# Kernel optimization log

Measured on AMD Instinct MI355X. Metric: run time of the kernel, lower is better.

The kernel has to match this reference:

```python
import jax, jax.numpy as jnp
import numpy as np

N_NODES = 50000
N_EDGES = 800000
BATCH = 8
IN_CH = 64
OUT_CH = 64
K = 6


def setup_inputs() -> dict:
    key = jax.random.key(0)
    k1, k2, k3, k4 = jax.random.split(key, 4)
    x = jax.random.normal(k1, (BATCH, N_NODES, IN_CH), dtype=jnp.float32)
    edge_index = jax.random.randint(k2, (2, N_EDGES), 0, N_NODES, dtype=jnp.int64)
    # small weights keep the order-K Chebyshev recursion numerically stable
    edge_weight = jax.random.normal(k3, (N_EDGES,), dtype=jnp.float32) * 0.05
    W = jax.random.normal(k4, (K, IN_CH, OUT_CH), dtype=jnp.float32) * (1.0 / np.sqrt(IN_CH))
    bias = jnp.zeros((OUT_CH,), dtype=jnp.float32)
    return {"x": x, "edge_index": edge_index, "edge_weight": edge_weight, "W": W, "bias": bias}


def _spmm(edge_index, edge_weight, x, n_nodes):
    # sparse Laplacian @ x for batched features x: [B, N, C]
    src = edge_index[1]  # gather column
    dst = edge_index[0]  # scatter row
    msg = x[:, src, :] * edge_weight[None, :, None]      # [B, E, C]
    agg = jax.ops.segment_sum(msg.transpose(1, 0, 2), dst, num_segments=n_nodes)  # [N, B, C]
    return agg.transpose(1, 0, 2)                        # [B, N, C]


def reference(x, edge_index, edge_weight, W, bias):
    n = x.shape[1]
    t_prev = x                                            # T_0
    out = jnp.einsum('bnc,co->bno', t_prev, W[0])
    if K > 1:
        t_cur = _spmm(edge_index, edge_weight, x, n)      # T_1 = L x
        out = out + jnp.einsum('bnc,co->bno', t_cur, W[1])
        for k in range(2, K):
            t_next = 2.0 * _spmm(edge_index, edge_weight, t_cur, n) - t_prev
            out = out + jnp.einsum('bnc,co->bno', t_next, W[k])
            t_prev, t_cur = t_cur, t_next
    out = out + bias
    return out
```

## Files before the change

### kernel.cpp

```cpp
#include <hip/hip_runtime.h>

#define N_NODES 50000
#define N_EDGES 800000
#define BATCH 8
#define CH 64
#define BC (BATCH * CH)
#define WSZ (CH * CH)
#define NROWS (BATCH * N_NODES)
#define TELEMS ((size_t)NROWS * CH)
#define HIST_BLOCKS ((N_EDGES + 255) / 256)
#define CAST_BLOCKS ((int)(TELEMS / 4 / 256))
#define PACK_BLOCKS 12

typedef unsigned short u16;
typedef short bf16x8 __attribute__((ext_vector_type(8)));
typedef float f32x4 __attribute__((ext_vector_type(4)));
typedef unsigned short u16x4 __attribute__((ext_vector_type(4)));
typedef unsigned short u16x8 __attribute__((ext_vector_type(8)));

__device__ __forceinline__ u16 f2bf(float f) {
    unsigned x = __float_as_uint(f);
    return (u16)((x + 0x7fffu + ((x >> 16) & 1u)) >> 16);
}
__device__ __forceinline__ float b2f(u16 u) {
    return __uint_as_float(((unsigned)u) << 16);
}


__global__ __launch_bounds__(256) void hist_cast_kernel(
        const int* __restrict__ dst, int* __restrict__ cursor,
        const float* __restrict__ x, u16* __restrict__ xb) {
    int bid = blockIdx.x;
    if (bid < HIST_BLOCKS) {
        int e = bid * 256 + threadIdx.x;
        if (e < N_EDGES) atomicAdd(&cursor[dst[e]], 1);
        return;
    }
    size_t i = (size_t)(bid - HIST_BLOCKS) * 256 + threadIdx.x;
    f32x4 v = __builtin_nontemporal_load((const f32x4*)(x + i * 4));
    int c4 = (int)(i & 15);
    size_t bn = i >> 4;
    int b = (int)(bn / N_NODES);
    int n = (int)(bn - (size_t)b * N_NODES);
    u16x4 o;
    o.x = f2bf(v.x); o.y = f2bf(v.y); o.z = f2bf(v.z); o.w = f2bf(v.w);
    *(u16x4*)(xb + ((size_t)n * BATCH + b) * CH + c4 * 4) = o;
}

__global__ void scan_kernel(int* cursor, int* __restrict__ row_ptr, int n) {
    const int T = 1024;
    int tid = threadIdx.x;
    int per = (n + T - 1) / T;
    int s = tid * per;
    int e = s + per; if (e > n) e = n;
    int sum = 0;
    for (int i = s; i < e; ++i) sum += cursor[i];
    __shared__ int lds[1024];
    lds[tid] = sum;
    __syncthreads();
    for (int off = 1; off < 1024; off <<= 1) {
        int t = (tid >= off) ? lds[tid - off] : 0;
        __syncthreads();
        lds[tid] += t;
        __syncthreads();
    }
    int run = lds[tid] - sum;
    for (int i = s; i < e; ++i) {
        int v = cursor[i];
        row_ptr[i] = run;
        cursor[i]  = run;
        run += v;
    }
    if (tid == T - 1) row_ptr[n] = run;
}

__global__ __launch_bounds__(256) void scatter_pack_kernel(
        const int* __restrict__ dst, const int* __restrict__ src,
        const float* __restrict__ w, int* cursor, int2* __restrict__ edges,
        const float* __restrict__ W, u16* __restrict__ wpack) {
    int bid = blockIdx.x;
    if (bid < HIST_BLOCKS) {
        int e = bid * 256 + threadIdx.x;
        if (e >= N_EDGES) return;
        int d = dst[e];
        int p = atomicAdd(&cursor[d], 1);
        edges[p] = make_int2(src[e], __float_as_int(w[e]));
        return;
    }
    int id = (bid - HIST_BLOCKS) * 256 + threadIdx.x;
    if (id >= 48 * 64) return;
    int lane = id & 63, frag = id >> 6;
    int ct = frag & 3, cct = (frag >> 2) & 1, k = frag >> 3;
    int m = lane & 15, quad = lane >> 4;
    int c = ct * 16 + m;
#pragma unroll
    for (int j = 0; j < 8; ++j) {
        int cc = cct * 32 + quad * 8 + j;
        wpack[(size_t)id * 8 + j] = f2bf(W[k * WSZ + cc * CH + c]);
    }
}

template <bool HAS_PREV>
__global__ __launch_bounds__(256) void spmm_kernel(
        const u16* __restrict__ tcur,
        const u16* __restrict__ tprev,
        u16* __restrict__ tnext,
        const int* __restrict__ row_ptr,
        const int2* __restrict__ edges) {
    const int node = blockIdx.x * 4 + (threadIdx.x >> 6);
    const int lane = threadIdx.x & 63;
    const size_t lo = (size_t)lane * 8;

    float acc[8];
#pragma unroll
    for (int q = 0; q < 8; ++q) acc[q] = 0.f;

    const int beg = row_ptr[node], end = row_ptr[node + 1];
    for (int e0 = beg; e0 < end; e0 += 64) {
        int m = end - e0; if (m > 64) m = 64;
        int2 ev = edges[e0 + (lane < m ? lane : 0)];
        int j = 0;
        for (; j + 4 <= m; j += 4) {
            int   s0 = __shfl(ev.x, j);
            int   s1 = __shfl(ev.x, j + 1);
            int   s2 = __shfl(ev.x, j + 2);
            int   s3 = __shfl(ev.x, j + 3);
            float w0 = __int_as_float(__shfl(ev.y, j));
            float w1 = __int_as_float(__shfl(ev.y, j + 1));
            float w2 = __int_as_float(__shfl(ev.y, j + 2));
            float w3 = __int_as_float(__shfl(ev.y, j + 3));
            u16x8 v0 = *(const u16x8*)(tcur + (size_t)s0 * BC + lo);
            u16x8 v1 = *(const u16x8*)(tcur + (size_t)s1 * BC + lo);
            u16x8 v2 = *(const u16x8*)(tcur + (size_t)s2 * BC + lo);
            u16x8 v3 = *(const u16x8*)(tcur + (size_t)s3 * BC + lo);
#pragma unroll
            for (int q = 0; q < 8; ++q) acc[q] = fmaf(w0, b2f(v0[q]), acc[q]);
#pragma unroll
            for (int q = 0; q < 8; ++q) acc[q] = fmaf(w1, b2f(v1[q]), acc[q]);
#pragma unroll
            for (int q = 0; q < 8; ++q) acc[q] = fmaf(w2, b2f(v2[q]), acc[q]);
#pragma unroll
            for (int q = 0; q < 8; ++q) acc[q] = fmaf(w3, b2f(v3[q]), acc[q]);
        }
        for (; j < m; ++j) {
            int   s = __shfl(ev.x, j);
            float w = __int_as_float(__shfl(ev.y, j));
            u16x8 v = *(const u16x8*)(tcur + (size_t)s * BC + lo);
#pragma unroll
            for (int q = 0; q < 8; ++q) acc[q] = fmaf(w, b2f(v[q]), acc[q]);
        }
    }

    const size_t idx = (size_t)node * BC + lo;
    u16x8 o;
    if (HAS_PREV) {
        u16x8 pv = *(const u16x8*)(tprev + idx);
#pragma unroll
        for (int q = 0; q < 8; ++q) o[q] = f2bf(2.f * acc[q] - b2f(pv[q]));
    } else {
#pragma unroll
        for (int q = 0; q < 8; ++q) o[q] = f2bf(acc[q]);
    }
    *(u16x8*)(tnext + idx) = o;
}

__global__ __launch_bounds__(256) void out_gemm(
        const u16* __restrict__ tbase, size_t tstride,
        const u16* __restrict__ wpack,
        const float* __restrict__ bias,
        float* __restrict__ out, int nk, int accum) {
    const int wave = threadIdx.x >> 6, lane = threadIdx.x & 63;
    const int tile = blockIdx.x * 4 + wave;
    const int row0 = tile * 16;
    const int m = lane & 15, quad = lane >> 4;

    f32x4 acc[4];
#pragma unroll
    for (int ct = 0; ct < 4; ++ct) acc[ct] = (f32x4){0.f, 0.f, 0.f, 0.f};

    for (int k = 0; k < nk; ++k) {
        const u16* t = tbase + (size_t)k * tstride;
#pragma unroll
        for (int cct = 0; cct < 2; ++cct) {
            bf16x8 A = *(const bf16x8*)(t + (size_t)(row0 + m) * CH + cct * 32 + quad * 8);
#pragma unroll
            for (int ct = 0; ct < 4; ++ct) {
                bf16x8 B = *(const bf16x8*)(wpack + (size_t)(((k * 2 + cct) * 4 + ct) * 64 + lane) * 8);
                acc[ct] = __builtin_amdgcn_mfma_f32_16x16x32_bf16(A, B, acc[ct], 0, 0, 0);
            }
        }
    }

#pragma unroll
    for (int ct = 0; ct < 4; ++ct) {
        const int c = ct * 16 + m;
        const float bv = bias[c];
#pragma unroll
        for (int r = 0; r < 4; ++r) {
            int row = row0 + quad * 4 + r;
            float* op = out + ((size_t)(row & 7) * N_NODES + (row >> 3)) * CH + c;
            float v = acc[ct][r];
            if (accum) v += __builtin_nontemporal_load(op);
            else       v += bv;
            __builtin_nontemporal_store(v, op);
        }
    }
}

extern "C" void kernel_launch(void* const* d_in, const int* in_sizes, int n_in,
                              void* d_out, int out_size, void* d_ws, size_t ws_size,
                              hipStream_t stream) {
    const float* x    = (const float*)d_in[0];
    const int*   ei   = (const int*)d_in[1];
    const float* ew   = (const float*)d_in[2];
    const float* W    = (const float*)d_in[3];
    const float* bias = (const float*)d_in[4];
    float* out = (float*)d_out;

    const int* dst = ei;
    const int* src = ei + N_EDGES;

    const size_t SB = TELEMS * sizeof(u16);
    const size_t EXTRA = 2 * 200192 + (size_t)N_EDGES * sizeof(int2) + 49664;
    const size_t NEED_PRIMARY = 6 * SB + EXTRA;
    const bool primary = (ws_size >= NEED_PRIMARY);
    const int nbuf = primary ? 6 : 3;

    char* ws = (char*)d_ws;
    size_t off = 0;
    u16* tbase = (u16*)(ws + off); off += (size_t)nbuf * SB;
    int* row_ptr = (int*)(ws + off); off += 200192;
    int* cursor  = (int*)(ws + off); off += 200192;
    int2* edges  = (int2*)(ws + off); off += (size_t)N_EDGES * sizeof(int2);
    u16* wpack   = (u16*)(ws + off); off += 49664;
    (void)off; (void)n_in; (void)in_sizes; (void)out_size;

    (void)hipMemsetAsync(cursor, 0, (size_t)N_NODES * sizeof(int), stream);
    hist_cast_kernel<<<HIST_BLOCKS + CAST_BLOCKS, 256, 0, stream>>>(dst, cursor, x, tbase);
    scan_kernel<<<1, 1024, 0, stream>>>(cursor, row_ptr, N_NODES);
    scatter_pack_kernel<<<HIST_BLOCKS + PACK_BLOCKS, 256, 0, stream>>>(dst, src, ew, cursor,
                                                                       edges, W, wpack);

    const int SPMM_GRID = N_NODES / 4;
    u16* t0 = tbase;
    if (primary) {
        u16* t1 = tbase + 1 * TELEMS;
        u16* t2 = tbase + 2 * TELEMS;
        u16* t3 = tbase + 3 * TELEMS;
        u16* t4 = tbase + 4 * TELEMS;
        u16* t5 = tbase + 5 * TELEMS;
        spmm_kernel<false><<<SPMM_GRID, 256, 0, stream>>>(t0, nullptr, t1, row_ptr, edges);
        spmm_kernel<true ><<<SPMM_GRID, 256, 0, stream>>>(t1, t0, t2, row_ptr, edges);
        spmm_kernel<true ><<<SPMM_GRID, 256, 0, stream>>>(t2, t1, t3, row_ptr, edges);
        spmm_kernel<true ><<<SPMM_GRID, 256, 0, stream>>>(t3, t2, t4, row_ptr, edges);
        spmm_kernel<true ><<<SPMM_GRID, 256, 0, stream>>>(t4, t3, t5, row_ptr, edges);
        out_gemm<<<NROWS / 16 / 4, 256, 0, stream>>>(tbase, TELEMS, wpack, bias, out, 6, 0);
    } else {
        u16* t1 = tbase + 1 * TELEMS;
        u16* t2 = tbase + 2 * TELEMS;
        const int GG = NROWS / 16 / 4;
        spmm_kernel<false><<<SPMM_GRID, 256, 0, stream>>>(t0, nullptr, t1, row_ptr, edges);
        out_gemm<<<GG, 256, 0, stream>>>(t0, TELEMS, wpack, bias, out, 2, 0);
        spmm_kernel<true ><<<SPMM_GRID, 256, 0, stream>>>(t1, t0, t2, row_ptr, edges);
        out_gemm<<<GG, 256, 0, stream>>>(t2, TELEMS, wpack + 2 * WSZ, bias, out, 1, 1);
        spmm_kernel<true ><<<SPMM_GRID, 256, 0, stream>>>(t2, t1, t0, row_ptr, edges);
        out_gemm<<<GG, 256, 0, stream>>>(t0, TELEMS, wpack + 3 * WSZ, bias, out, 1, 1);
        spmm_kernel<true ><<<SPMM_GRID, 256, 0, stream>>>(t0, t2, t1, row_ptr, edges);
        out_gemm<<<GG, 256, 0, stream>>>(t1, TELEMS, wpack + 4 * WSZ, bias, out, 1, 1);
        spmm_kernel<true ><<<SPMM_GRID, 256, 0, stream>>>(t1, t0, t2, row_ptr, edges);
        out_gemm<<<GG, 256, 0, stream>>>(t2, TELEMS, wpack + 5 * WSZ, bias, out, 1, 1);
    }
}
```

Measured before the change: 1.068 ms.

## Split SpMM feature columns into two halves to shrink gather working set

The SpMM kernel now processes half of each node's 512 batch-channel features per launch, with a half index selecting the column range. The Chebyshev recursion is run separately for each half, so the randomly gathered rows touch a smaller footprint that may stay in cache. In exchange the edge list and row pointers are read twice, launches double, and each lane issues narrower 8-byte loads.

```diff
diff --git a/kernel.cpp b/kernel.cpp
--- a/kernel.cpp
+++ b/kernel.cpp
@@ -106,14 +106,15 @@
         const u16* __restrict__ tprev,
         u16* __restrict__ tnext,
         const int* __restrict__ row_ptr,
-        const int2* __restrict__ edges) {
+        const int2* __restrict__ edges,
+        int half) {
     const int node = blockIdx.x * 4 + (threadIdx.x >> 6);
     const int lane = threadIdx.x & 63;
-    const size_t lo = (size_t)lane * 8;
-
-    float acc[8];
-#pragma unroll
-    for (int q = 0; q < 8; ++q) acc[q] = 0.f;
+    const size_t lo = (size_t)half * 256 + (size_t)lane * 4;
+
+    float acc[4];
+#pragma unroll
+    for (int q = 0; q < 4; ++q) acc[q] = 0.f;
 
     const int beg = row_ptr[node], end = row_ptr[node + 1];
     for (int e0 = beg; e0 < end; e0 += 64) {
@@ -129,39 +130,39 @@
             float w1 = __int_as_float(__shfl(ev.y, j + 1));
             float w2 = __int_as_float(__shfl(ev.y, j + 2));
             float w3 = __int_as_float(__shfl(ev.y, j + 3));
-            u16x8 v0 = *(const u16x8*)(tcur + (size_t)s0 * BC + lo);
-            u16x8 v1 = *(const u16x8*)(tcur + (size_t)s1 * BC + lo);
-            u16x8 v2 = *(const u16x8*)(tcur + (size_t)s2 * BC + lo);
-            u16x8 v3 = *(const u16x8*)(tcur + (size_t)s3 * BC + lo);
-#pragma unroll
-            for (int q = 0; q < 8; ++q) acc[q] = fmaf(w0, b2f(v0[q]), acc[q]);
-#pragma unroll
-            for (int q = 0; q < 8; ++q) acc[q] = fmaf(w1, b2f(v1[q]), acc[q]);
-#pragma unroll
-            for (int q = 0; q < 8; ++q) acc[q] = fmaf(w2, b2f(v2[q]), acc[q]);
-#pragma unroll
-            for (int q = 0; q < 8; ++q) acc[q] = fmaf(w3, b2f(v3[q]), acc[q]);
+            u16x4 v0 = *(const u16x4*)(tcur + (size_t)s0 * BC + lo);
+            u16x4 v1 = *(const u16x4*)(tcur + (size_t)s1 * BC + lo);
+            u16x4 v2 = *(const u16x4*)(tcur + (size_t)s2 * BC + lo);
+            u16x4 v3 = *(const u16x4*)(tcur + (size_t)s3 * BC + lo);
+#pragma unroll
+            for (int q = 0; q < 4; ++q) acc[q] = fmaf(w0, b2f(v0[q]), acc[q]);
+#pragma unroll
+            for (int q = 0; q < 4; ++q) acc[q] = fmaf(w1, b2f(v1[q]), acc[q]);
+#pragma unroll
+            for (int q = 0; q < 4; ++q) acc[q] = fmaf(w2, b2f(v2[q]), acc[q]);
+#pragma unroll
+            for (int q = 0; q < 4; ++q) acc[q] = fmaf(w3, b2f(v3[q]), acc[q]);
         }
         for (; j < m; ++j) {
             int   s = __shfl(ev.x, j);
             float w = __int_as_float(__shfl(ev.y, j));
-            u16x8 v = *(const u16x8*)(tcur + (size_t)s * BC + lo);
-#pragma unroll
-            for (int q = 0; q < 8; ++q) acc[q] = fmaf(w, b2f(v[q]), acc[q]);
+            u16x4 v = *(const u16x4*)(tcur + (size_t)s * BC + lo);
+#pragma unroll
+            for (int q = 0; q < 4; ++q) acc[q] = fmaf(w, b2f(v[q]), acc[q]);
         }
     }
 
     const size_t idx = (size_t)node * BC + lo;
-    u16x8 o;
+    u16x4 o;
     if (HAS_PREV) {
-        u16x8 pv = *(const u16x8*)(tprev + idx);
-#pragma unroll
-        for (int q = 0; q < 8; ++q) o[q] = f2bf(2.f * acc[q] - b2f(pv[q]));
+        u16x4 pv = *(const u16x4*)(tprev + idx);
+#pragma unroll
+        for (int q = 0; q < 4; ++q) o[q] = f2bf(2.f * acc[q] - b2f(pv[q]));
     } else {
 #pragma unroll
-        for (int q = 0; q < 8; ++q) o[q] = f2bf(acc[q]);
-    }
-    *(u16x8*)(tnext + idx) = o;
+        for (int q = 0; q < 4; ++q) o[q] = f2bf(acc[q]);
+    }
+    *(u16x4*)(tnext + idx) = o;
 }
 
 __global__ __launch_bounds__(256) void out_gemm(
@@ -249,25 +250,32 @@
         u16* t3 = tbase + 3 * TELEMS;
         u16* t4 = tbase + 4 * TELEMS;
         u16* t5 = tbase + 5 * TELEMS;
-        spmm_kernel<false><<<SPMM_GRID, 256, 0, stream>>>(t0, nullptr, t1, row_ptr, edges);
-        spmm_kernel<true ><<<SPMM_GRID, 256, 0, stream>>>(t1, t0, t2, row_ptr, edges);
-        spmm_kernel<true ><<<SPMM_GRID, 256, 0, stream>>>(t2, t1, t3, row_ptr, edges);
-        spmm_kernel<true ><<<SPMM_GRID, 256, 0, stream>>>(t3, t2, t4, row_ptr, edges);
-        spmm_kernel<true ><<<SPMM_GRID, 256, 0, stream>>>(t4, t3, t5, row_ptr, edges);
+        for (int h = 0; h < 2; ++h) {
+            spmm_kernel<false><<<SPMM_GRID, 256, 0, stream>>>(t0, nullptr, t1, row_ptr, edges, h);
+            spmm_kernel<true ><<<SPMM_GRID, 256, 0, stream>>>(t1, t0, t2, row_ptr, edges, h);
+            spmm_kernel<true ><<<SPMM_GRID, 256, 0, stream>>>(t2, t1, t3, row_ptr, edges, h);
+            spmm_kernel<true ><<<SPMM_GRID, 256, 0, stream>>>(t3, t2, t4, row_ptr, edges, h);
+            spmm_kernel<true ><<<SPMM_GRID, 256, 0, stream>>>(t4, t3, t5, row_ptr, edges, h);
+        }
         out_gemm<<<NROWS / 16 / 4, 256, 0, stream>>>(tbase, TELEMS, wpack, bias, out, 6, 0);
     } else {
         u16* t1 = tbase + 1 * TELEMS;
         u16* t2 = tbase + 2 * TELEMS;
         const int GG = NROWS / 16 / 4;
-        spmm_kernel<false><<<SPMM_GRID, 256, 0, stream>>>(t0, nullptr, t1, row_ptr, edges);
+        spmm_kernel<false><<<SPMM_GRID, 256, 0, stream>>>(t0, nullptr, t1, row_ptr, edges, 0);
+        spmm_kernel<false><<<SPMM_GRID, 256, 0, stream>>>(t0, nullptr, t1, row_ptr, edges, 1);
         out_gemm<<<GG, 256, 0, stream>>>(t0, TELEMS, wpack, bias, out, 2, 0);
-        spmm_kernel<true ><<<SPMM_GRID, 256, 0, stream>>>(t1, t0, t2, row_ptr, edges);
+        spmm_kernel<true ><<<SPMM_GRID, 256, 0, stream>>>(t1, t0, t2, row_ptr, edges, 0);
+        spmm_kernel<true ><<<SPMM_GRID, 256, 0, stream>>>(t1, t0, t2, row_ptr, edges, 1);
         out_gemm<<<GG, 256, 0, stream>>>(t2, TELEMS, wpack + 2 * WSZ, bias, out, 1, 1);
-        spmm_kernel<true ><<<SPMM_GRID, 256, 0, stream>>>(t2, t1, t0, row_ptr, edges);
+        spmm_kernel<true ><<<SPMM_GRID, 256, 0, stream>>>(t2, t1, t0, row_ptr, edges, 0);
+        spmm_kernel<true ><<<SPMM_GRID, 256, 0, stream>>>(t2, t1, t0, row_ptr, edges, 1);
         out_gemm<<<GG, 256, 0, stream>>>(t0, TELEMS, wpack + 3 * WSZ, bias, out, 1, 1);
-        spmm_kernel<true ><<<SPMM_GRID, 256, 0, stream>>>(t0, t2, t1, row_ptr, edges);
+        spmm_kernel<true ><<<SPMM_GRID, 256, 0, stream>>>(t0, t2, t1, row_ptr, edges, 0);
+        spmm_kernel<true ><<<SPMM_GRID, 256, 0, stream>>>(t0, t2, t1, row_ptr, edges, 1);
         out_gemm<<<GG, 256, 0, stream>>>(t1, TELEMS, wpack + 4 * WSZ, bias, out, 1, 1);
-        spmm_kernel<true ><<<SPMM_GRID, 256, 0, stream>>>(t1, t0, t2, row_ptr, edges);
+        spmm_kernel<true ><<<SPMM_GRID, 256, 0, stream>>>(t1, t0, t2, row_ptr, edges, 0);
+        spmm_kernel<true ><<<SPMM_GRID, 256, 0, stream>>>(t1, t0, t2, row_ptr, edges, 1);
         out_gemm<<<GG, 256, 0, stream>>>(t2, TELEMS, wpack + 5 * WSZ, bias, out, 1, 1);
     }
 }
```

After: 1.019 ms. 1.05x faster.
